# Kernel tuning notes

Measured on AMD Instinct MI355X. Metric: run time of the kernel, lower is better.

Reference implementation:

```python
import jax, jax.numpy as jnp
import numpy as np

B, S, DIM = 2, 2048, 4096
NH, NKV, HD = 32, 8, 128
RANK, ALPHA = 16, 32
THETA = 500000.0
SCALE = ALPHA / RANK  # 2.0


def setup_inputs() -> dict:
    key = jax.random.key(0)
    ks = jax.random.split(key, 14)
    s = 0.02  # init scale for numerical stability
    inp = {
        "x": jax.random.normal(ks[0], (B, S, DIM), jnp.float32),
        "w_q": jax.random.normal(ks[1], (NH * HD, DIM), jnp.float32) * s,
        "w_k": jax.random.normal(ks[2], (NKV * HD, DIM), jnp.float32) * s,
        "w_v": jax.random.normal(ks[3], (NKV * HD, DIM), jnp.float32) * s,
        "w_o": jax.random.normal(ks[4], (DIM, NH * HD), jnp.float32) * s,
        "lora_wq_a": jax.random.normal(ks[5], (RANK, DIM), jnp.float32) * s,
        "lora_wq_b": jax.random.normal(ks[6], (NH * HD, RANK), jnp.float32) * s,
        "lora_wk_a": jax.random.normal(ks[7], (RANK, DIM), jnp.float32) * s,
        "lora_wk_b": jax.random.normal(ks[8], (NKV * HD, RANK), jnp.float32) * s,
        "lora_wv_a": jax.random.normal(ks[9], (RANK, DIM), jnp.float32) * s,
        "lora_wv_b": jax.random.normal(ks[10], (NKV * HD, RANK), jnp.float32) * s,
        "lora_wo_a": jax.random.normal(ks[11], (RANK, DIM), jnp.float32) * s,
        "lora_wo_b": jax.random.normal(ks[12], (DIM, RANK), jnp.float32) * s,
        "cache_k": jnp.zeros((B, S, NKV, HD), jnp.float32),
        "cache_v": jnp.zeros((B, S, NKV, HD), jnp.float32),
    }
    # rotary frequencies: freqs_cis = exp(i * t * theta^{-2j/hd}), shape (S, HD//2)
    inv_freq = 1.0 / (THETA ** (np.arange(0, HD, 2, dtype=np.float32) / HD))
    t = np.arange(S, dtype=np.float32)
    freqs = np.outer(t, inv_freq)
    inp["freqs_cos"] = jnp.asarray(np.cos(freqs))
    inp["freqs_sin"] = jnp.asarray(np.sin(freqs))
    # causal mask (prefill)
    inp["mask"] = jnp.triu(jnp.full((S, S), -1e9, jnp.float32), 1)
    inp["start_pos"] = 0
    return inp


def _apply_rope(t, cos, sin):
    # t: [b, s, h, d]; cos/sin: [s, d//2] -> complex rotation on (even, odd) pairs
    b, s, h, d = t.shape
    t2 = t.reshape(b, s, h, d // 2, 2)
    tr, ti = t2[..., 0], t2[..., 1]
    c = cos[None, :, None, :]
    sn = sin[None, :, None, :]
    out = jnp.stack([tr * c - ti * sn, tr * sn + ti * c], axis=-1)
    return out.reshape(b, s, h, d)


def reference(x, w_q, w_k, w_v, w_o,
              lora_wq_a, lora_wq_b, lora_wk_a, lora_wk_b,
              lora_wv_a, lora_wv_b, lora_wo_a, lora_wo_b,
              cache_k, cache_v, freqs_cos, freqs_sin, mask, start_pos):
    bsz, seqlen, _ = x.shape
    n_rep = NH // NKV

    xq = x @ w_q.T + SCALE * ((x @ lora_wq_a.T) @ lora_wq_b.T)
    xk = x @ w_k.T + SCALE * ((x @ lora_wk_a.T) @ lora_wk_b.T)
    xv = x @ w_v.T + SCALE * ((x @ lora_wv_a.T) @ lora_wv_b.T)

    xq = xq.reshape(bsz, seqlen, NH, HD)
    xk = xk.reshape(bsz, seqlen, NKV, HD)
    xv = xv.reshape(bsz, seqlen, NKV, HD)

    xq = _apply_rope(xq, freqs_cos, freqs_sin)
    xk = _apply_rope(xk, freqs_cos, freqs_sin)

    # KV-cache write + read of [:start_pos+seqlen]
    cache_k = jax.lax.dynamic_update_slice(cache_k, xk, (0, start_pos, 0, 0))
    cache_v = jax.lax.dynamic_update_slice(cache_v, xv, (0, start_pos, 0, 0))
    kv_len = start_pos + seqlen
    keys = cache_k[:, :kv_len]      # [b, k, nkv, hd]
    values = cache_v[:, :kv_len]

    # GQA expansion (repeat_interleave on head axis)
    keys = jnp.repeat(keys, n_rep, axis=2)    # [b, k, nh, hd]
    values = jnp.repeat(values, n_rep, axis=2)

    scores = jnp.einsum("bqhd,bkhd->bhqk", xq, keys) / jnp.sqrt(jnp.float32(HD))
    scores = scores + mask[None, None, :, :]
    probs = jax.nn.softmax(scores.astype(jnp.float32), axis=-1).astype(xq.dtype)
    out = jnp.einsum("bhqk,bkhd->bqhd", probs, values).reshape(bsz, seqlen, NH * HD)

    # NOTE: the original applies the output LoRA to x (not to out) -- kept faithful.
    return out @ w_o.T + SCALE * ((x @ lora_wo_a.T) @ lora_wo_b.T)
```

## Files before the change

### kernel.cpp

```cpp
#include <hip/hip_runtime.h>


typedef __attribute__((ext_vector_type(8))) short short8;
typedef __attribute__((ext_vector_type(4))) short short4v;
typedef __attribute__((ext_vector_type(4))) float f32x4;

#define LORA_SCALE 2.0f
#define INV_SQRT_HD 0.08838834764831845f

static __device__ __forceinline__ unsigned short f2bf(float f) {
  union { float f; unsigned int u; } v; v.f = f;
  unsigned int r = (v.u + 0x7fffu + ((v.u >> 16) & 1u)) >> 16;
  return (unsigned short)r;
}
static __device__ __forceinline__ float bf2f(unsigned short h) {
  union { unsigned int u; float f; } v; v.u = ((unsigned int)h) << 16;
  return v.f;
}

#define GL16(src, dst) __builtin_amdgcn_global_load_lds( \
    (const unsigned int __attribute__((address_space(1)))*)(src), \
    (unsigned int __attribute__((address_space(3)))*)(dst), 16, 0, 0)

template <int BF16OUT>
__global__ __launch_bounds__(512, 2) void gemm256_kernel(
    const unsigned short* __restrict__ A,
    const unsigned short* __restrict__ B,
    void* __restrict__ C, int K, int ldc, int T)
{
  __shared__ unsigned short As[2][2][8192];
  __shared__ unsigned short Bs[2][2][8192];
  const int tid = threadIdx.x;
  const int w = tid >> 6, l = tid & 63;
  const int l15 = l & 15, lhi = l >> 4;
  const int m0 = blockIdx.y * 256, n0 = blockIdx.x * 256;
  const int wm = (w >> 2) * 128, wn = (w & 3) * 64;

  const f32x4 vz = {0.f, 0.f, 0.f, 0.f};
  f32x4 acc[8][4];
#pragma unroll
  for (int i = 0; i < 8; ++i)
#pragma unroll
    for (int j = 0; j < 4; ++j) acc[i][j] = vz;

  const int srow = tid >> 2, sg = tid & 3;
  const int sgsw = sg ^ ((tid >> 3) & 3);
  const unsigned short* gA = A + (size_t)(m0 + srow) * K + sgsw * 8;
  const unsigned short* gB = B + (size_t)(n0 + srow) * K + sgsw * 8;
  const size_t rK = (size_t)128 * K;
  const int ld0 = srow * 32 + sg * 8;

#define STAGE_A(buf, kh, kb) do { \
    GL16(gA + (kb) + (kh) * 32, &As[buf][kh][ld0]); \
    GL16(gA + rK + (kb) + (kh) * 32, &As[buf][kh][4096 + ld0]); } while (0)
#define STAGE_B(buf, kh, kb) do { \
    GL16(gB + (kb) + (kh) * 32, &Bs[buf][kh][ld0]); \
    GL16(gB + rK + (kb) + (kh) * 32, &Bs[buf][kh][4096 + ld0]); } while (0)
#define LDA8(buf, kc) do { \
    _Pragma("unroll") for (int mi = 0; mi < 8; ++mi) { \
      int r = wm + mi * 16 + l15; \
      af[mi] = *(const short8*)&As[buf][kc][r * 32 + ((lhi ^ ((r >> 1) & 3)) << 3)]; } } while (0)
#define LDB1(buf, kc, ni) \
    (*(const short8*)&Bs[buf][kc][(wn + (ni) * 16 + l15) * 32 + \
        ((lhi ^ (((wn + (ni) * 16 + l15) >> 1) & 3)) << 3)])
#define MM16(bx, by, cx, cy) do { \
    __builtin_amdgcn_s_setprio(1); \
    _Pragma("unroll") for (int mi = 0; mi < 8; ++mi) { \
      acc[mi][cx] = __builtin_amdgcn_mfma_f32_16x16x32_bf16(af[mi], bx, acc[mi][cx], 0, 0, 0); \
      acc[mi][cy] = __builtin_amdgcn_mfma_f32_16x16x32_bf16(af[mi], by, acc[mi][cy], 0, 0, 0); } \
    __builtin_amdgcn_s_setprio(0); } while (0)
#define VMC4() asm volatile("s_waitcnt vmcnt(4)" ::: "memory")
#define VMC0() asm volatile("s_waitcnt vmcnt(0)" ::: "memory")
#define BARX() __builtin_amdgcn_s_barrier()

  STAGE_A(0, 0, 0); STAGE_B(0, 0, 0); STAGE_A(0, 1, 0); STAGE_B(0, 1, 0);
  VMC4(); BARX();

  short8 af[8], b0, b1, b2, b3;
  for (int t = 0; t < T - 1; ++t) {
    const int cur = t & 1, nxt = cur ^ 1;
    const int kb = (t + 1) * 64;
    LDA8(cur, 0);
    b0 = LDB1(cur, 0, 0); b1 = LDB1(cur, 0, 1);
    STAGE_A(nxt, 0, kb);
    BARX();
    MM16(b0, b1, 0, 1);
    b2 = LDB1(cur, 0, 2); b3 = LDB1(cur, 0, 3);
    STAGE_B(nxt, 0, kb);
    VMC4(); BARX();
    MM16(b2, b3, 2, 3);
    LDA8(cur, 1);
    b0 = LDB1(cur, 1, 0); b1 = LDB1(cur, 1, 1);
    STAGE_A(nxt, 1, kb);
    BARX();
    MM16(b0, b1, 0, 1);
    b2 = LDB1(cur, 1, 2); b3 = LDB1(cur, 1, 3);
    STAGE_B(nxt, 1, kb);
    VMC4(); BARX();
    MM16(b2, b3, 2, 3);
  }
  {
    const int cur = (T - 1) & 1;
    LDA8(cur, 0);
    b0 = LDB1(cur, 0, 0); b1 = LDB1(cur, 0, 1);
    BARX();
    MM16(b0, b1, 0, 1);
    b2 = LDB1(cur, 0, 2); b3 = LDB1(cur, 0, 3);
    VMC0(); BARX();
    MM16(b2, b3, 2, 3);
    LDA8(cur, 1);
    b0 = LDB1(cur, 1, 0); b1 = LDB1(cur, 1, 1);
    MM16(b0, b1, 0, 1);
    b2 = LDB1(cur, 1, 2); b3 = LDB1(cur, 1, 3);
    MM16(b2, b3, 2, 3);
  }
#pragma unroll
  for (int mi = 0; mi < 8; ++mi)
#pragma unroll
    for (int ni = 0; ni < 4; ++ni)
#pragma unroll
      for (int j = 0; j < 4; ++j) {
        size_t row = (size_t)(m0 + wm + mi * 16 + lhi * 4 + j);
        size_t col = (size_t)(n0 + wn + ni * 16 + l15);
        if (BF16OUT) ((unsigned short*)C)[row * ldc + col] = f2bf(acc[mi][ni][j]);
        else         ((float*)C)[row * ldc + col] = acc[mi][ni][j];
      }
#undef STAGE_A
#undef STAGE_B
#undef LDA8
#undef LDB1
#undef MM16
#undef VMC4
#undef VMC0
#undef BARX
}

__global__ __launch_bounds__(256, 2) void flash_kernel(
    const unsigned short* __restrict__ qkv,
    unsigned short* __restrict__ outA)
{
  __shared__ unsigned short Ks[64 * 128];
  __shared__ unsigned short Vt[128 * 64];
  __shared__ unsigned short Ps[4][32 * 64];
  const int tid = threadIdx.x;
  const int w = tid >> 6, l = tid & 63;
  const int l15 = l & 15, lhi = l >> 4;
  const int qt = 15 - blockIdx.x;
  const int h = blockIdx.y, b = blockIdx.z;
  const int q0 = qt * 128;
  const int qw0 = q0 + w * 32;
  const int kh = h >> 2;
  const size_t rowb = (size_t)b * 2048;

  short8 qf[2][4];
#pragma unroll
  for (int mf = 0; mf < 2; ++mf)
#pragma unroll
    for (int kc = 0; kc < 4; ++kc)
      qf[mf][kc] = *(const short8*)&qkv[(rowb + qw0 + mf * 16 + l15) * 6144 + h * 128 + kc * 32 + lhi * 8];

  const f32x4 vzero = {0.f, 0.f, 0.f, 0.f};
  f32x4 po[2][8];
  float mrun[2][4], lrun[2][4];
#pragma unroll
  for (int mf = 0; mf < 2; ++mf) {
#pragma unroll
    for (int df = 0; df < 8; ++df) po[mf][df] = vzero;
#pragma unroll
    for (int j = 0; j < 4; ++j) { mrun[mf][j] = -1e30f; lrun[mf][j] = 0.f; }
  }

  const int vrg = tid >> 4;
  const int vg  = tid & 15;

  const int nt = (q0 >> 6) + 2;
  for (int t = 0; t < nt; ++t) {
    const int kv0 = t * 64;
#pragma unroll
    for (int it = 0; it < 4; ++it) {
      int idx = it * 256 + tid;
      int r = idx >> 4, g = idx & 15;
      const size_t gro = (rowb + kv0 + r) * 6144 + kh * 128 + g * 8;
      *(short8*)&Ks[r * 128 + ((g * 8) ^ ((r & 7) << 3))] = *(const short8*)&qkv[gro + 4096];
    }
    {
      short8 v0, v1, v2, v3;
      const size_t vb = (rowb + kv0 + vrg * 4) * 6144 + kh * 128 + vg * 8 + 5120;
      v0 = *(const short8*)&qkv[vb];
      v1 = *(const short8*)&qkv[vb + 6144];
      v2 = *(const short8*)&qkv[vb + 12288];
      v3 = *(const short8*)&qkv[vb + 18432];
#pragma unroll
      for (int e = 0; e < 8; ++e) {
        int d = vg * 8 + e;
        int sv = ((d & 7) ^ ((d >> 3) & 7)) << 3;
        short4v o; o[0] = v0[e]; o[1] = v1[e]; o[2] = v2[e]; o[3] = v3[e];
        *(short4v*)&Vt[d * 64 + ((vrg * 4) ^ sv)] = o;
      }
    }
    __syncthreads();
    if (kv0 <= qw0 + 31) {
      f32x4 sa[2][4];
#pragma unroll
      for (int mf = 0; mf < 2; ++mf)
#pragma unroll
        for (int nf = 0; nf < 4; ++nf) sa[mf][nf] = vzero;
      __builtin_amdgcn_s_setprio(1);
#pragma unroll
      for (int kc = 0; kc < 4; ++kc) {
        short8 kf[4];
#pragma unroll
        for (int nf = 0; nf < 4; ++nf) {
          int row = nf * 16 + l15;
          kf[nf] = *(const short8*)&Ks[row * 128 + ((kc * 32 + lhi * 8) ^ ((row & 7) << 3))];
        }
#pragma unroll
        for (int mf = 0; mf < 2; ++mf)
#pragma unroll
          for (int nf = 0; nf < 4; ++nf)
            sa[mf][nf] = __builtin_amdgcn_mfma_f32_16x16x32_bf16(qf[mf][kc], kf[nf], sa[mf][nf], 0, 0, 0);
      }
      __builtin_amdgcn_s_setprio(0);
      const bool diag = (kv0 + 63) > qw0;
#pragma unroll
      for (int mf = 0; mf < 2; ++mf) {
#pragma unroll
        for (int nf = 0; nf < 4; ++nf)
#pragma unroll
          for (int j = 0; j < 4; ++j) {
            float v = sa[mf][nf][j] * INV_SQRT_HD;
            if (diag) {
              int kvc = kv0 + nf * 16 + l15;
              int qr  = qw0 + mf * 16 + lhi * 4 + j;
              if (kvc > qr) v = -1e30f;
            }
            sa[mf][nf][j] = v;
          }
#pragma unroll
        for (int j = 0; j < 4; ++j) {
          float rm = fmaxf(fmaxf(sa[mf][0][j], sa[mf][1][j]), fmaxf(sa[mf][2][j], sa[mf][3][j]));
#pragma unroll
          for (int d = 1; d < 16; d <<= 1) rm = fmaxf(rm, __shfl_xor(rm, d));
          float mnew = fmaxf(mrun[mf][j], rm);
          float sc = __expf(mrun[mf][j] - mnew);
          float rs = 0.f;
#pragma unroll
          for (int nf = 0; nf < 4; ++nf) {
            float p = __expf(sa[mf][nf][j] - mnew);
            sa[mf][nf][j] = p;
            rs += p;
          }
#pragma unroll
          for (int d = 1; d < 16; d <<= 1) rs += __shfl_xor(rs, d);
          lrun[mf][j] = lrun[mf][j] * sc + rs;
          mrun[mf][j] = mnew;
#pragma unroll
          for (int df = 0; df < 8; ++df) po[mf][df][j] *= sc;
        }
#pragma unroll
        for (int j = 0; j < 4; ++j) {
          int q = mf * 16 + lhi * 4 + j;
          int sq = (q & 7) << 3;
#pragma unroll
          for (int nf = 0; nf < 4; ++nf)
            Ps[w][q * 64 + ((nf * 16 + l15) ^ sq)] = f2bf(sa[mf][nf][j]);
        }
      }
      __builtin_amdgcn_s_setprio(1);
#pragma unroll
      for (int kc2 = 0; kc2 < 2; ++kc2) {
        short8 pf[2];
#pragma unroll
        for (int mf = 0; mf < 2; ++mf) {
          int q = mf * 16 + l15;
          pf[mf] = *(const short8*)&Ps[w][q * 64 + ((kc2 * 32 + lhi * 8) ^ ((q & 7) << 3))];
        }
#pragma unroll
        for (int df = 0; df < 8; ++df) {
          int d = df * 16 + l15;
          int sv = ((d & 7) ^ ((d >> 3) & 7)) << 3;
          short8 vf = *(const short8*)&Vt[d * 64 + ((kc2 * 32 + lhi * 8) ^ sv)];
#pragma unroll
          for (int mf = 0; mf < 2; ++mf)
            po[mf][df] = __builtin_amdgcn_mfma_f32_16x16x32_bf16(pf[mf], vf, po[mf][df], 0, 0, 0);
        }
      }
      __builtin_amdgcn_s_setprio(0);
    }
    __syncthreads();
  }
#pragma unroll
  for (int mf = 0; mf < 2; ++mf)
#pragma unroll
    for (int df = 0; df < 8; ++df)
#pragma unroll
      for (int j = 0; j < 4; ++j) {
        size_t q = (size_t)(qw0 + mf * 16 + lhi * 4 + j);
        int d = df * 16 + l15;
        outA[(rowb + q) * 4160 + h * 128 + d] = f2bf(po[mf][df][j] / lrun[mf][j]);
      }
}

__global__ void convert_x_kernel(const float* __restrict__ x, unsigned short* __restrict__ Xb)
{
  int idx = blockIdx.x * 256 + threadIdx.x;
  int m = idx >> 9;
  int c8 = (idx & 511) * 8;
  f32x4 a = *(const f32x4*)&x[(size_t)m * 4096 + c8];
  f32x4 b2 = *(const f32x4*)&x[(size_t)m * 4096 + c8 + 4];
  short8 o;
#pragma unroll
  for (int e = 0; e < 4; ++e) { o[e] = (short)f2bf(a[e]); o[4 + e] = (short)f2bf(b2[e]); }
  *(short8*)&Xb[(size_t)m * 4096 + c8] = o;
}

__global__ __launch_bounds__(256) void fold_kernel(
    const float* __restrict__ w, const float* __restrict__ b,
    const float* __restrict__ a, unsigned short* __restrict__ W)
{
  __shared__ unsigned short als[16][512];
  const int tid = threadIdx.x;
  const int n0 = blockIdx.x * 8;
  const int c0 = blockIdx.y * 512;
#pragma unroll
  for (int it = 0; it < 8; ++it) {
    int flat = it * 1024 + tid * 4;
    int r = flat >> 9, c = flat & 511;
    f32x4 v = *(const f32x4*)&a[(size_t)r * 4096 + c0 + c];
    short4v o;
#pragma unroll
    for (int e = 0; e < 4; ++e) o[e] = (short)f2bf(LORA_SCALE * v[e]);
    *(short4v*)&als[r][c] = o;
  }
  __syncthreads();
  const int n = n0 + (tid >> 5);
  const int cb = (tid & 31) * 16;
  const float* wrow = w + (size_t)n * 4096 + c0 + cb;
  const float* brow = b + (size_t)n * 16;
  float bb[16];
#pragma unroll
  for (int r4 = 0; r4 < 4; ++r4) {
    f32x4 t = *(const f32x4*)&brow[r4 * 4];
#pragma unroll
    for (int e = 0; e < 4; ++e) bb[r4 * 4 + e] = t[e];
  }
  float acc[16];
#pragma unroll
  for (int j4 = 0; j4 < 4; ++j4) {
    f32x4 t = *(const f32x4*)&wrow[j4 * 4];
#pragma unroll
    for (int e = 0; e < 4; ++e) acc[j4 * 4 + e] = t[e];
  }
#pragma unroll
  for (int r = 0; r < 16; ++r) {
    short8 a0 = *(const short8*)&als[r][cb];
    short8 a1 = *(const short8*)&als[r][cb + 8];
    float br = bb[r];
#pragma unroll
    for (int e = 0; e < 8; ++e) {
      acc[e]     += br * bf2f((unsigned short)a0[e]);
      acc[8 + e] += br * bf2f((unsigned short)a1[e]);
    }
  }
  short8 o0, o1;
#pragma unroll
  for (int e = 0; e < 8; ++e) { o0[e] = (short)f2bf(acc[e]); o1[e] = (short)f2bf(acc[8 + e]); }
  unsigned short* dst = W + (size_t)n * 4096 + c0 + cb;
  *(short8*)&dst[0] = o0;
  *(short8*)&dst[8] = o1;
}

__global__ void build_wo_kernel(const float* __restrict__ wo, const float* __restrict__ bo,
                                unsigned short* __restrict__ W)
{
  int idx = blockIdx.x * 256 + threadIdx.x;
  int n = idx / 520;
  int c8 = (idx - n * 520) * 8;
  short8 o;
  if (c8 < 4096) {
    const float* src = wo + (size_t)n * 4096 + c8;
    f32x4 a = *(const f32x4*)&src[0];
    f32x4 b2 = *(const f32x4*)&src[4];
#pragma unroll
    for (int e = 0; e < 4; ++e) { o[e] = (short)f2bf(a[e]); o[4 + e] = (short)f2bf(b2[e]); }
  } else {
#pragma unroll
    for (int e = 0; e < 8; ++e) {
      int j = c8 + e - 4096;
      float v = (j < 16) ? bo[(size_t)n * 16 + j] : 0.f;
      o[e] = (short)f2bf(v);
    }
  }
  *(short8*)&W[(size_t)n * 4160 + c8] = o;
}

__global__ __launch_bounds__(256) void t_kernel(
    const float* __restrict__ x, const float* __restrict__ ao, float* __restrict__ t)
{
  __shared__ float red[4][16];
  const int m = blockIdx.x;
  const int tid = threadIdx.x;
  const int w = tid >> 6, l = tid & 63;
  float part[16];
#pragma unroll
  for (int r = 0; r < 16; ++r) part[r] = 0.f;
#pragma unroll
  for (int it = 0; it < 4; ++it) {
    int k = it * 1024 + tid * 4;
    f32x4 xv = *(const f32x4*)&x[(size_t)m * 4096 + k];
#pragma unroll
    for (int r = 0; r < 16; ++r) {
      f32x4 av = *(const f32x4*)&ao[(size_t)r * 4096 + k];
      part[r] += xv[0] * av[0] + xv[1] * av[1] + xv[2] * av[2] + xv[3] * av[3];
    }
  }
#pragma unroll
  for (int d = 1; d < 64; d <<= 1)
#pragma unroll
    for (int r = 0; r < 16; ++r) part[r] += __shfl_xor(part[r], d);
  if (l == 0)
#pragma unroll
    for (int r = 0; r < 16; ++r) red[w][r] = part[r];
  __syncthreads();
  if (tid < 16)
    t[(size_t)m * 16 + tid] = red[0][tid] + red[1][tid] + red[2][tid] + red[3][tid];
}

__global__ void a_tail_kernel(const float* __restrict__ t, unsigned short* __restrict__ Ao)
{
  int m = blockIdx.x * 256 + threadIdx.x;
  const float* src = t + (size_t)m * 16;
  unsigned short* d = Ao + (size_t)m * 4160 + 4096;
  short8 o0, o1, z;
#pragma unroll
  for (int e = 0; e < 8; ++e) {
    o0[e] = (short)f2bf(LORA_SCALE * src[e]);
    o1[e] = (short)f2bf(LORA_SCALE * src[8 + e]);
    z[e] = 0;
  }
  *(short8*)&d[0] = o0;
  *(short8*)&d[8] = o1;
#pragma unroll
  for (int c = 0; c < 6; ++c) *(short8*)&d[16 + c * 8] = z;
}

__global__ void rope_kernel(unsigned short* __restrict__ qkv,
                            const float* __restrict__ fcos,
                            const float* __restrict__ fsin)
{
  int idx = blockIdx.x * 256 + threadIdx.x;
  int m = idx / 640;
  int c8 = (idx - m * 640) * 8;
  int s = m & 2047;
  int i0 = (c8 & 127) >> 1;
  unsigned short* p = qkv + (size_t)m * 6144 + c8;
  short8 v = *(short8*)p;
  f32x4 c = *(const f32x4*)&fcos[s * 64 + i0];
  f32x4 sn = *(const f32x4*)&fsin[s * 64 + i0];
  short8 o;
#pragma unroll
  for (int pr = 0; pr < 4; ++pr) {
    float re = bf2f((unsigned short)v[2 * pr]);
    float im = bf2f((unsigned short)v[2 * pr + 1]);
    o[2 * pr]     = (short)f2bf(re * c[pr] - im * sn[pr]);
    o[2 * pr + 1] = (short)f2bf(re * sn[pr] + im * c[pr]);
  }
  *(short8*)p = o;
}

extern "C" void kernel_launch(void* const* d_in, const int* in_sizes, int n_in,
                              void* d_out, int out_size, void* d_ws, size_t ws_size,
                              hipStream_t stream) {
  (void)in_sizes; (void)n_in; (void)out_size; (void)ws_size;
  const float* x    = (const float*)d_in[0];
  const float* w_q  = (const float*)d_in[1];
  const float* w_k  = (const float*)d_in[2];
  const float* w_v  = (const float*)d_in[3];
  const float* w_o  = (const float*)d_in[4];
  const float* la_q = (const float*)d_in[5];
  const float* lb_q = (const float*)d_in[6];
  const float* la_k = (const float*)d_in[7];
  const float* lb_k = (const float*)d_in[8];
  const float* la_v = (const float*)d_in[9];
  const float* lb_v = (const float*)d_in[10];
  const float* la_o = (const float*)d_in[11];
  const float* lb_o = (const float*)d_in[12];
  const float* fcos = (const float*)d_in[15];
  const float* fsin = (const float*)d_in[16];

  unsigned short* Wqkv = (unsigned short*)d_ws;
  unsigned short* Wo   = Wqkv + (size_t)6144 * 4096;
  unsigned short* Xbf  = Wo + (size_t)4096 * 4160;
  unsigned short* QKV  = Xbf + (size_t)4096 * 4096;
  unsigned short* Ao   = QKV + (size_t)4096 * 6144;
  float* t             = (float*)(Ao + (size_t)4096 * 4160);

  dim3 blk(256);
  fold_kernel<<<dim3(512, 8), blk, 0, stream>>>(w_q, lb_q, la_q, Wqkv);
  fold_kernel<<<dim3(128, 8), blk, 0, stream>>>(w_k, lb_k, la_k, Wqkv + (size_t)4096 * 4096);
  fold_kernel<<<dim3(128, 8), blk, 0, stream>>>(w_v, lb_v, la_v, Wqkv + (size_t)5120 * 4096);
  build_wo_kernel<<<8320, blk, 0, stream>>>(w_o, lb_o, Wo);
  convert_x_kernel<<<8192, blk, 0, stream>>>(x, Xbf);
  t_kernel<<<4096, blk, 0, stream>>>(x, la_o, t);
  a_tail_kernel<<<16, blk, 0, stream>>>(t, Ao);
  gemm256_kernel<1><<<dim3(24, 16), dim3(512), 0, stream>>>(Xbf, Wqkv, QKV, 4096, 6144, 64);
  rope_kernel<<<10240, blk, 0, stream>>>(QKV, fcos, fsin);
  flash_kernel<<<dim3(16, 32, 2), blk, 0, stream>>>(QKV, Ao);
  gemm256_kernel<0><<<dim3(16, 16), dim3(512), 0, stream>>>(Ao, Wo, d_out, 4160, 4096, 65);
}
```

Before: 775.9 us.

## Double-buffer K/V tiles in flash attention with async LDS loads

The flash attention kernel now keeps two LDS buffers for K and transposed V. It prefetches the next tile's K through global_load_lds and holds the next V rows in registers while computing on the current tile. The transposed V is written to LDS after compute, so each iteration needs one barrier instead of two. This hides global load latency behind the MFMA work, at the cost of twice the LDS for K/V (about 64KB plus P), which may lower occupancy below 2 blocks per CU, and extra registers for the V prefetch.

```diff
diff --git a/kernel.cpp b/kernel.cpp
--- a/kernel.cpp
+++ b/kernel.cpp
@@ -139,8 +139,8 @@
     const unsigned short* __restrict__ qkv,
     unsigned short* __restrict__ outA)
 {
-  __shared__ unsigned short Ks[64 * 128];
-  __shared__ unsigned short Vt[128 * 64];
+  __shared__ unsigned short Ks[2][64 * 128];
+  __shared__ unsigned short Vt[2][128 * 64];
   __shared__ unsigned short Ps[4][32 * 64];
   const int tid = threadIdx.x;
   const int w = tid >> 6, l = tid & 63;
@@ -170,35 +170,47 @@
     for (int j = 0; j < 4; ++j) { mrun[mf][j] = -1e30f; lrun[mf][j] = 0.f; }
   }
 
+  const int krh = 4 * w + (l >> 4);
+  const int kg8 = (l & 15) * 8;
   const int vrg = tid >> 4;
   const int vg  = tid & 15;
+
+  short8 v0, v1, v2, v3;
+
+#define STAGE_K(buf, kv0) do { \
+    _Pragma("unroll") for (int it = 0; it < 4; ++it) { \
+      int r = it * 16 + krh; \
+      GL16(&qkv[(rowb + (kv0) + r) * 6144 + 4096 + kh * 128 + (kg8 ^ ((r & 7) << 3))], \
+           &Ks[buf][(it * 16 + 4 * w) * 128]); \
+    } } while (0)
+#define LOAD_V(kv0) do { \
+    const size_t vb_ = (rowb + (kv0) + vrg * 4) * 6144 + kh * 128 + vg * 8 + 5120; \
+    v0 = *(const short8*)&qkv[vb_]; \
+    v1 = *(const short8*)&qkv[vb_ + 6144]; \
+    v2 = *(const short8*)&qkv[vb_ + 12288]; \
+    v3 = *(const short8*)&qkv[vb_ + 18432]; } while (0)
+#define WRITE_VT(buf) do { \
+    _Pragma("unroll") for (int e = 0; e < 8; ++e) { \
+      int d = vg * 8 + e; \
+      int sv = ((d & 7) ^ ((d >> 3) & 7)) << 3; \
+      short4v o_; o_[0] = v0[e]; o_[1] = v1[e]; o_[2] = v2[e]; o_[3] = v3[e]; \
+      *(short4v*)&Vt[buf][d * 64 + ((vrg * 4) ^ sv)] = o_; \
+    } } while (0)
+
+  STAGE_K(0, 0);
+  LOAD_V(0);
+  WRITE_VT(0);
+  __syncthreads();
 
   const int nt = (q0 >> 6) + 2;
   for (int t = 0; t < nt; ++t) {
     const int kv0 = t * 64;
-#pragma unroll
-    for (int it = 0; it < 4; ++it) {
-      int idx = it * 256 + tid;
-      int r = idx >> 4, g = idx & 15;
-      const size_t gro = (rowb + kv0 + r) * 6144 + kh * 128 + g * 8;
-      *(short8*)&Ks[r * 128 + ((g * 8) ^ ((r & 7) << 3))] = *(const short8*)&qkv[gro + 4096];
+    const int cur = t & 1, nxt = cur ^ 1;
+    const bool pf = (t + 1) < nt;
+    if (pf) {
+      STAGE_K(nxt, kv0 + 64);
+      LOAD_V(kv0 + 64);
     }
-    {
-      short8 v0, v1, v2, v3;
-      const size_t vb = (rowb + kv0 + vrg * 4) * 6144 + kh * 128 + vg * 8 + 5120;
-      v0 = *(const short8*)&qkv[vb];
-      v1 = *(const short8*)&qkv[vb + 6144];
-      v2 = *(const short8*)&qkv[vb + 12288];
-      v3 = *(const short8*)&qkv[vb + 18432];
-#pragma unroll
-      for (int e = 0; e < 8; ++e) {
-        int d = vg * 8 + e;
-        int sv = ((d & 7) ^ ((d >> 3) & 7)) << 3;
-        short4v o; o[0] = v0[e]; o[1] = v1[e]; o[2] = v2[e]; o[3] = v3[e];
-        *(short4v*)&Vt[d * 64 + ((vrg * 4) ^ sv)] = o;
-      }
-    }
-    __syncthreads();
     if (kv0 <= qw0 + 31) {
       f32x4 sa[2][4];
 #pragma unroll
@@ -212,7 +224,7 @@
 #pragma unroll
         for (int nf = 0; nf < 4; ++nf) {
           int row = nf * 16 + l15;
-          kf[nf] = *(const short8*)&Ks[row * 128 + ((kc * 32 + lhi * 8) ^ ((row & 7) << 3))];
+          kf[nf] = *(const short8*)&Ks[cur][row * 128 + ((kc * 32 + lhi * 8) ^ ((row & 7) << 3))];
         }
 #pragma unroll
         for (int mf = 0; mf < 2; ++mf)
@@ -269,26 +281,30 @@
       __builtin_amdgcn_s_setprio(1);
 #pragma unroll
       for (int kc2 = 0; kc2 < 2; ++kc2) {
-        short8 pf[2];
+        short8 pf2[2];
 #pragma unroll
         for (int mf = 0; mf < 2; ++mf) {
           int q = mf * 16 + l15;
-          pf[mf] = *(const short8*)&Ps[w][q * 64 + ((kc2 * 32 + lhi * 8) ^ ((q & 7) << 3))];
+          pf2[mf] = *(const short8*)&Ps[w][q * 64 + ((kc2 * 32 + lhi * 8) ^ ((q & 7) << 3))];
         }
 #pragma unroll
         for (int df = 0; df < 8; ++df) {
           int d = df * 16 + l15;
           int sv = ((d & 7) ^ ((d >> 3) & 7)) << 3;
-          short8 vf = *(const short8*)&Vt[d * 64 + ((kc2 * 32 + lhi * 8) ^ sv)];
+          short8 vf = *(const short8*)&Vt[cur][d * 64 + ((kc2 * 32 + lhi * 8) ^ sv)];
 #pragma unroll
           for (int mf = 0; mf < 2; ++mf)
-            po[mf][df] = __builtin_amdgcn_mfma_f32_16x16x32_bf16(pf[mf], vf, po[mf][df], 0, 0, 0);
+            po[mf][df] = __builtin_amdgcn_mfma_f32_16x16x32_bf16(pf2[mf], vf, po[mf][df], 0, 0, 0);
         }
       }
       __builtin_amdgcn_s_setprio(0);
     }
+    if (pf) WRITE_VT(nxt);
     __syncthreads();
   }
+#undef STAGE_K
+#undef LOAD_V
+#undef WRITE_VT
 #pragma unroll
   for (int mf = 0; mf < 2; ++mf)
 #pragma unroll
```

Measured after the change: 894.2 us. 1.15x slower.

## Pair causal query tiles per flash block to balance work and share K/V loads

Applied to the files above, without the earlier changes.

Each flash-attention block now handles two query tiles, p and 15-p, so every block does the same amount of causal work. The K/V tiles staged in shared memory are reused by both query tiles, and the grid shrinks from 16 to 8 in x, giving 512 blocks. The intent is to remove load imbalance and cut redundant K/V global loads. In exchange, registers per thread roughly double because of the two accumulator sets, which could lower occupancy or cause spills under launch_bounds(256,2).

```diff
diff --git a/kernel.cpp b/kernel.cpp
--- a/kernel.cpp
+++ b/kernel.cpp
@@ -21,6 +21,10 @@
 #define GL16(src, dst) __builtin_amdgcn_global_load_lds( \
     (const unsigned int __attribute__((address_space(1)))*)(src), \
     (unsigned int __attribute__((address_space(3)))*)(dst), 16, 0, 0)
+
+#define VMC4() asm volatile("s_waitcnt vmcnt(4)" ::: "memory")
+#define VMC0() asm volatile("s_waitcnt vmcnt(0)" ::: "memory")
+#define BARX() __builtin_amdgcn_s_barrier()
 
 template <int BF16OUT>
 __global__ __launch_bounds__(512, 2) void gemm256_kernel(
@@ -69,9 +73,6 @@
       acc[mi][cx] = __builtin_amdgcn_mfma_f32_16x16x32_bf16(af[mi], bx, acc[mi][cx], 0, 0, 0); \
       acc[mi][cy] = __builtin_amdgcn_mfma_f32_16x16x32_bf16(af[mi], by, acc[mi][cy], 0, 0, 0); } \
     __builtin_amdgcn_s_setprio(0); } while (0)
-#define VMC4() asm volatile("s_waitcnt vmcnt(4)" ::: "memory")
-#define VMC0() asm volatile("s_waitcnt vmcnt(0)" ::: "memory")
-#define BARX() __builtin_amdgcn_s_barrier()
 
   STAGE_A(0, 0, 0); STAGE_B(0, 0, 0); STAGE_A(0, 1, 0); STAGE_B(0, 1, 0);
   VMC4(); BARX();
@@ -130,9 +131,103 @@
 #undef LDA8
 #undef LDB1
 #undef MM16
-#undef VMC4
-#undef VMC0
-#undef BARX
+}
+
+__device__ __forceinline__ void flash_tile(
+    const unsigned short* __restrict__ Ks,
+    const unsigned short* __restrict__ Vt,
+    unsigned short* __restrict__ Psw,
+    const short8 (&qf)[2][4], f32x4 (&po)[2][8],
+    float (&mrun)[2][4], float (&lrun)[2][4],
+    int kv0, int qw0, int l15, int lhi)
+{
+  const f32x4 vzero = {0.f, 0.f, 0.f, 0.f};
+  f32x4 sa[2][4];
+#pragma unroll
+  for (int mf = 0; mf < 2; ++mf)
+#pragma unroll
+    for (int nf = 0; nf < 4; ++nf) sa[mf][nf] = vzero;
+  __builtin_amdgcn_s_setprio(1);
+#pragma unroll
+  for (int kc = 0; kc < 4; ++kc) {
+    short8 kf[4];
+#pragma unroll
+    for (int nf = 0; nf < 4; ++nf) {
+      int row = nf * 16 + l15;
+      kf[nf] = *(const short8*)&Ks[row * 128 + ((kc * 32 + lhi * 8) ^ ((row & 7) << 3))];
+    }
+#pragma unroll
+    for (int mf = 0; mf < 2; ++mf)
+#pragma unroll
+      for (int nf = 0; nf < 4; ++nf)
+        sa[mf][nf] = __builtin_amdgcn_mfma_f32_16x16x32_bf16(qf[mf][kc], kf[nf], sa[mf][nf], 0, 0, 0);
+  }
+  __builtin_amdgcn_s_setprio(0);
+  const bool diag = (kv0 + 63) > qw0;
+#pragma unroll
+  for (int mf = 0; mf < 2; ++mf) {
+#pragma unroll
+    for (int nf = 0; nf < 4; ++nf)
+#pragma unroll
+      for (int j = 0; j < 4; ++j) {
+        float v = sa[mf][nf][j] * INV_SQRT_HD;
+        if (diag) {
+          int kvc = kv0 + nf * 16 + l15;
+          int qr  = qw0 + mf * 16 + lhi * 4 + j;
+          if (kvc > qr) v = -1e30f;
+        }
+        sa[mf][nf][j] = v;
+      }
+#pragma unroll
+    for (int j = 0; j < 4; ++j) {
+      float rm = fmaxf(fmaxf(sa[mf][0][j], sa[mf][1][j]), fmaxf(sa[mf][2][j], sa[mf][3][j]));
+#pragma unroll
+      for (int d = 1; d < 16; d <<= 1) rm = fmaxf(rm, __shfl_xor(rm, d));
+      float mnew = fmaxf(mrun[mf][j], rm);
+      float sc = __expf(mrun[mf][j] - mnew);
+      float rs = 0.f;
+#pragma unroll
+      for (int nf = 0; nf < 4; ++nf) {
+        float p = __expf(sa[mf][nf][j] - mnew);
+        sa[mf][nf][j] = p;
+        rs += p;
+      }
+#pragma unroll
+      for (int d = 1; d < 16; d <<= 1) rs += __shfl_xor(rs, d);
+      lrun[mf][j] = lrun[mf][j] * sc + rs;
+      mrun[mf][j] = mnew;
+#pragma unroll
+      for (int df = 0; df < 8; ++df) po[mf][df][j] *= sc;
+    }
+#pragma unroll
+    for (int j = 0; j < 4; ++j) {
+      int q = mf * 16 + lhi * 4 + j;
+      int sq = (q & 7) << 3;
+#pragma unroll
+      for (int nf = 0; nf < 4; ++nf)
+        Psw[q * 64 + ((nf * 16 + l15) ^ sq)] = f2bf(sa[mf][nf][j]);
+    }
+  }
+  __builtin_amdgcn_s_setprio(1);
+#pragma unroll
+  for (int kc2 = 0; kc2 < 2; ++kc2) {
+    short8 pf[2];
+#pragma unroll
+    for (int mf = 0; mf < 2; ++mf) {
+      int q = mf * 16 + l15;
+      pf[mf] = *(const short8*)&Psw[q * 64 + ((kc2 * 32 + lhi * 8) ^ ((q & 7) << 3))];
+    }
+#pragma unroll
+    for (int df = 0; df < 8; ++df) {
+      int d = df * 16 + l15;
+      int sv = ((d & 7) ^ ((d >> 3) & 7)) << 3;
+      short8 vf = *(const short8*)&Vt[d * 64 + ((kc2 * 32 + lhi * 8) ^ sv)];
+#pragma unroll
+      for (int mf = 0; mf < 2; ++mf)
+        po[mf][df] = __builtin_amdgcn_mfma_f32_16x16x32_bf16(pf[mf], vf, po[mf][df], 0, 0, 0);
+    }
+  }
+  __builtin_amdgcn_s_setprio(0);
 }
 
 __global__ __launch_bounds__(256, 2) void flash_kernel(
@@ -145,35 +240,41 @@
   const int tid = threadIdx.x;
   const int w = tid >> 6, l = tid & 63;
   const int l15 = l & 15, lhi = l >> 4;
-  const int qt = 15 - blockIdx.x;
+  const int p = blockIdx.x;
+  const int qta = p, qtb = 15 - p;
   const int h = blockIdx.y, b = blockIdx.z;
-  const int q0 = qt * 128;
-  const int qw0 = q0 + w * 32;
+  const int qwa = qta * 128 + w * 32;
+  const int qwb = qtb * 128 + w * 32;
   const int kh = h >> 2;
   const size_t rowb = (size_t)b * 2048;
 
-  short8 qf[2][4];
+  short8 qfa[2][4], qfb[2][4];
 #pragma unroll
   for (int mf = 0; mf < 2; ++mf)
 #pragma unroll
-    for (int kc = 0; kc < 4; ++kc)
-      qf[mf][kc] = *(const short8*)&qkv[(rowb + qw0 + mf * 16 + l15) * 6144 + h * 128 + kc * 32 + lhi * 8];
+    for (int kc = 0; kc < 4; ++kc) {
+      qfa[mf][kc] = *(const short8*)&qkv[(rowb + qwa + mf * 16 + l15) * 6144 + h * 128 + kc * 32 + lhi * 8];
+      qfb[mf][kc] = *(const short8*)&qkv[(rowb + qwb + mf * 16 + l15) * 6144 + h * 128 + kc * 32 + lhi * 8];
+    }
 
   const f32x4 vzero = {0.f, 0.f, 0.f, 0.f};
-  f32x4 po[2][8];
-  float mrun[2][4], lrun[2][4];
+  f32x4 poa[2][8], pob[2][8];
+  float mra[2][4], lra[2][4], mrb[2][4], lrb[2][4];
 #pragma unroll
   for (int mf = 0; mf < 2; ++mf) {
 #pragma unroll
-    for (int df = 0; df < 8; ++df) po[mf][df] = vzero;
-#pragma unroll
-    for (int j = 0; j < 4; ++j) { mrun[mf][j] = -1e30f; lrun[mf][j] = 0.f; }
+    for (int df = 0; df < 8; ++df) { poa[mf][df] = vzero; pob[mf][df] = vzero; }
+#pragma unroll
+    for (int j = 0; j < 4; ++j) {
+      mra[mf][j] = -1e30f; lra[mf][j] = 0.f;
+      mrb[mf][j] = -1e30f; lrb[mf][j] = 0.f;
+    }
   }
 
   const int vrg = tid >> 4;
   const int vg  = tid & 15;
 
-  const int nt = (q0 >> 6) + 2;
+  const int nt = 2 * qtb + 2;
   for (int t = 0; t < nt; ++t) {
     const int kv0 = t * 64;
 #pragma unroll
@@ -199,94 +300,10 @@
       }
     }
     __syncthreads();
-    if (kv0 <= qw0 + 31) {
-      f32x4 sa[2][4];
-#pragma unroll
-      for (int mf = 0; mf < 2; ++mf)
-#pragma unroll
-        for (int nf = 0; nf < 4; ++nf) sa[mf][nf] = vzero;
-      __builtin_amdgcn_s_setprio(1);
-#pragma unroll
-      for (int kc = 0; kc < 4; ++kc) {
-        short8 kf[4];
-#pragma unroll
-        for (int nf = 0; nf < 4; ++nf) {
-          int row = nf * 16 + l15;
-          kf[nf] = *(const short8*)&Ks[row * 128 + ((kc * 32 + lhi * 8) ^ ((row & 7) << 3))];
-        }
-#pragma unroll
-        for (int mf = 0; mf < 2; ++mf)
-#pragma unroll
-          for (int nf = 0; nf < 4; ++nf)
-            sa[mf][nf] = __builtin_amdgcn_mfma_f32_16x16x32_bf16(qf[mf][kc], kf[nf], sa[mf][nf], 0, 0, 0);
-      }
-      __builtin_amdgcn_s_setprio(0);
-      const bool diag = (kv0 + 63) > qw0;
-#pragma unroll
-      for (int mf = 0; mf < 2; ++mf) {
-#pragma unroll
-        for (int nf = 0; nf < 4; ++nf)
-#pragma unroll
-          for (int j = 0; j < 4; ++j) {
-            float v = sa[mf][nf][j] * INV_SQRT_HD;
-            if (diag) {
-              int kvc = kv0 + nf * 16 + l15;
-              int qr  = qw0 + mf * 16 + lhi * 4 + j;
-              if (kvc > qr) v = -1e30f;
-            }
-            sa[mf][nf][j] = v;
-          }
-#pragma unroll
-        for (int j = 0; j < 4; ++j) {
-          float rm = fmaxf(fmaxf(sa[mf][0][j], sa[mf][1][j]), fmaxf(sa[mf][2][j], sa[mf][3][j]));
-#pragma unroll
-          for (int d = 1; d < 16; d <<= 1) rm = fmaxf(rm, __shfl_xor(rm, d));
-          float mnew = fmaxf(mrun[mf][j], rm);
-          float sc = __expf(mrun[mf][j] - mnew);
-          float rs = 0.f;
-#pragma unroll
-          for (int nf = 0; nf < 4; ++nf) {
-            float p = __expf(sa[mf][nf][j] - mnew);
-            sa[mf][nf][j] = p;
-            rs += p;
-          }
-#pragma unroll
-          for (int d = 1; d < 16; d <<= 1) rs += __shfl_xor(rs, d);
-          lrun[mf][j] = lrun[mf][j] * sc + rs;
-          mrun[mf][j] = mnew;
-#pragma unroll
-          for (int df = 0; df < 8; ++df) po[mf][df][j] *= sc;
-        }
-#pragma unroll
-        for (int j = 0; j < 4; ++j) {
-          int q = mf * 16 + lhi * 4 + j;
-          int sq = (q & 7) << 3;
-#pragma unroll
-          for (int nf = 0; nf < 4; ++nf)
-            Ps[w][q * 64 + ((nf * 16 + l15) ^ sq)] = f2bf(sa[mf][nf][j]);
-        }
-      }
-      __builtin_amdgcn_s_setprio(1);
-#pragma unroll
-      for (int kc2 = 0; kc2 < 2; ++kc2) {
-        short8 pf[2];
-#pragma unroll
-        for (int mf = 0; mf < 2; ++mf) {
-          int q = mf * 16 + l15;
-          pf[mf] = *(const short8*)&Ps[w][q * 64 + ((kc2 * 32 + lhi * 8) ^ ((q & 7) << 3))];
-        }
-#pragma unroll
-        for (int df = 0; df < 8; ++df) {
-          int d = df * 16 + l15;
-          int sv = ((d & 7) ^ ((d >> 3) & 7)) << 3;
-          short8 vf = *(const short8*)&Vt[d * 64 + ((kc2 * 32 + lhi * 8) ^ sv)];
-#pragma unroll
-          for (int mf = 0; mf < 2; ++mf)
-            po[mf][df] = __builtin_amdgcn_mfma_f32_16x16x32_bf16(pf[mf], vf, po[mf][df], 0, 0, 0);
-        }
-      }
-      __builtin_amdgcn_s_setprio(0);
-    }
+    if (kv0 <= qwa + 31)
+      flash_tile(Ks, Vt, Ps[w], qfa, poa, mra, lra, kv0, qwa, l15, lhi);
+    if (kv0 <= qwb + 31)
+      flash_tile(Ks, Vt, Ps[w], qfb, pob, mrb, lrb, kv0, qwb, l15, lhi);
     __syncthreads();
   }
 #pragma unroll
@@ -295,9 +312,11 @@
     for (int df = 0; df < 8; ++df)
 #pragma unroll
       for (int j = 0; j < 4; ++j) {
-        size_t q = (size_t)(qw0 + mf * 16 + lhi * 4 + j);
         int d = df * 16 + l15;
-        outA[(rowb + q) * 4160 + h * 128 + d] = f2bf(po[mf][df][j] / lrun[mf][j]);
+        size_t qa = (size_t)(qwa + mf * 16 + lhi * 4 + j);
+        outA[(rowb + qa) * 4160 + h * 128 + d] = f2bf(poa[mf][df][j] / lra[mf][j]);
+        size_t qb = (size_t)(qwb + mf * 16 + lhi * 4 + j);
+        outA[(rowb + qb) * 4160 + h * 128 + d] = f2bf(pob[mf][df][j] / lrb[mf][j]);
       }
 }
 
@@ -505,6 +524,6 @@
   a_tail_kernel<<<16, blk, 0, stream>>>(t, Ao);
   gemm256_kernel<1><<<dim3(24, 16), dim3(512), 0, stream>>>(Xbf, Wqkv, QKV, 4096, 6144, 64);
   rope_kernel<<<10240, blk, 0, stream>>>(QKV, fcos, fsin);
-  flash_kernel<<<dim3(16, 32, 2), blk, 0, stream>>>(QKV, Ao);
+  flash_kernel<<<dim3(8, 32, 2), blk, 0, stream>>>(QKV, Ao);
   gemm256_kernel<0><<<dim3(16, 16), dim3(512), 0, stream>>>(Ao, Wo, d_out, 4160, 4096, 65);
 }
```

Result: slower. 1.190 ms (+53.4%).
